# Optimization experiments

Hardware: AMD Instinct MI355X
Metric: run time of the kernel (lower is better)

Reference implementation:

```python
import jax, jax.numpy as jnp
import numpy as np

NUM_RADII, NUM_THETA = 3, 16
RADIUS = 40.0
DT = 0.1
RELU_SHIFT = 0.2
B, N, NB, T_ENC, OTHER_CH = 4, 512, 512, 16, 3


def _rot_mats():
    # bin-center angles of the num_theta angular bins
    t = (jnp.arange(NUM_THETA, dtype=jnp.float32) + 0.5) * (2.0 * jnp.pi / NUM_THETA) - jnp.pi
    c, s = jnp.cos(t), jnp.sin(t)
    return jnp.stack([jnp.stack([c, -s], -1), jnp.stack([s, c], -1)], -2)  # [T,2,2]


def _steer_kernel(W):
    # W: [R,T,O,I,2,2]; equivariant steering K[r,t] = R(theta_t) W[r,t] R(theta_t)^T
    Rm = _rot_mats()
    K = jnp.einsum('tab,rtoibc,tdc->rtoiad', Rm, W, Rm)
    return K.reshape(NUM_RADII * NUM_THETA, W.shape[2], W.shape[3], 2, 2)  # [K,O,I,2,2]


def _equi_conv(src_pos, qry_pos, feats, mask, W):
    # src_pos [B,S,2], qry_pos [B,Q,2], feats [B,S,I,2] vector features, mask [B,Q,S]
    rel = src_pos[:, None, :, :] - qry_pos[:, :, None, :]          # [B,Q,S,2]
    d2 = jnp.sum(rel * rel, -1)
    dist = jnp.sqrt(d2 + 1e-9)
    theta = jnp.arctan2(rel[..., 1], rel[..., 0])
    rb = jnp.clip((dist / RADIUS * NUM_RADII).astype(jnp.int32), 0, NUM_RADII - 1)
    tb = jnp.mod(jnp.floor((theta + jnp.pi) / (2.0 * jnp.pi) * NUM_THETA).astype(jnp.int32), NUM_THETA)
    kidx = rb * NUM_THETA + tb                                     # [B,Q,S] polar bin id
    win = jnp.maximum(1.0 - d2 / (RADIUS * RADIUS), 0.0) ** 3      # smooth radial window
    w = win * mask
    H = jax.nn.one_hot(kidx, NUM_RADII * NUM_THETA, dtype=feats.dtype) * w[..., None]  # [B,Q,S,K]
    M = jnp.einsum('bqsk,bsiv->bqkiv', H, feats)                   # bin-accumulated neighbor features
    K = _steer_kernel(W)
    return jnp.einsum('bqkiv,koiuv->bqou', M, K)                   # [B,Q,O,2]


def _equi_linear(f, A, Bm):
    # rotation-equivariant linear on vector channels: (a*I + b*J) per (out,in)
    Jf = jnp.stack([-f[..., 1], f[..., 0]], -1)
    return jnp.einsum('oi,bniv->bnov', A, f) + jnp.einsum('oi,bniv->bnov', Bm, Jf)


def _forward(p0_enc, v0_enc, p0, v0, a, other_feats, box, box_feats, fluid_mask, box_mask,
             W_cf, W_co, A_df, B_df, layer_params):
    # update_pos_vel
    v1 = v0 + DT * a
    p1 = p0 + DT * (v0 + v1) * 0.5
    # forward(): feats = cat(other_feats, v0_enc) on channel dim -2
    feats = jnp.concatenate([other_feats, v0_enc], -2)
    # compute_correction
    fluid_feats = jnp.concatenate([v1[:, :, None, :], feats], -2)  # [B,N,20,2]
    out_conv_fluid = _equi_conv(p1, p1, fluid_feats, fluid_mask, W_cf)
    out_dense_fluid = _equi_linear(fluid_feats, A_df, B_df)
    out_conv_obst = _equi_conv(box, p1, box_feats[:, :, None, :], box_mask, W_co)
    output = jnp.concatenate([out_conv_obst, out_conv_fluid, out_dense_fluid], -2)  # [B,N,48,2]
    for (Wc, Ad, Bd) in layer_params:
        mags = (jnp.sum(output * output, -1) + 1e-6)[..., None]
        in_feats = output / mags * jax.nn.relu(mags - RELU_SHIFT)
        oc = _equi_conv(p1, p1, in_feats, fluid_mask, Wc)
        od = _equi_linear(in_feats, Ad, Bd)
        if od.shape[-2] == output.shape[-2]:
            output = oc + od + output
        else:
            output = oc + od
    corr = output / 128.0                                          # [B,N,1,2]
    # apply_correction
    p_corrected = p1 + corr[..., 0, :]
    v_corrected = (p_corrected - p0) / DT
    return p_corrected, v_corrected


def setup_inputs():
    key = jax.random.key(0)
    ks = jax.random.split(key, 32)
    d = {}
    d['p0_enc'] = jax.random.normal(ks[0], (B, N, T_ENC, 2), jnp.float32)
    d['v0_enc'] = jax.random.normal(ks[1], (B, N, T_ENC, 2), jnp.float32)
    d['p0'] = jax.random.uniform(ks[2], (B, N, 2), jnp.float32) * 100.0
    d['v0'] = jax.random.normal(ks[3], (B, N, 2), jnp.float32)
    d['a'] = jax.random.normal(ks[4], (B, N, 2), jnp.float32)
    d['other_feats'] = jax.random.normal(ks[5], (B, N, OTHER_CH, 2), jnp.float32)
    d['box'] = jax.random.uniform(ks[6], (B, NB, 2), jnp.float32) * 100.0
    d['box_feats'] = jax.random.normal(ks[7], (B, NB, 2), jnp.float32)
    d['fluid_mask'] = (jax.random.uniform(ks[8], (B, N, N)) < 0.5).astype(jnp.float32)
    d['box_mask'] = (jax.random.uniform(ks[9], (B, N, NB)) < 0.5).astype(jnp.float32)
    sc = 0.05
    d['W_cf'] = sc * jax.random.normal(ks[10], (NUM_RADII, NUM_THETA, 16, 20, 2, 2), jnp.float32)
    d['W_co'] = sc * jax.random.normal(ks[11], (NUM_RADII, NUM_THETA, 16, 1, 2, 2), jnp.float32)
    d['A_df'] = sc * jax.random.normal(ks[12], (16, 20), jnp.float32)
    d['B_df'] = sc * jax.random.normal(ks[13], (16, 20), jnp.float32)
    chans = [(32, 48), (32, 32), (32, 32), (1, 32)]
    for i, (o, ci) in enumerate(chans, start=1):
        d['W_c%d' % i] = sc * jax.random.normal(ks[13 + 3 * i], (NUM_RADII, NUM_THETA, o, ci, 2, 2), jnp.float32)
        d['A_d%d' % i] = sc * jax.random.normal(ks[14 + 3 * i], (o, ci), jnp.float32)
        d['B_d%d' % i] = sc * jax.random.normal(ks[15 + 3 * i], (o, ci), jnp.float32)
    return d


def reference(p0_enc, v0_enc, p0, v0, a, other_feats, box, box_feats, fluid_mask, box_mask,
              W_cf, W_co, A_df, B_df, W_c1, A_d1, B_d1, W_c2, A_d2, B_d2,
              W_c3, A_d3, B_d3, W_c4, A_d4, B_d4):
    layer_params = [(W_c1, A_d1, B_d1), (W_c2, A_d2, B_d2), (W_c3, A_d3, B_d3), (W_c4, A_d4, B_d4)]
    return _forward(p0_enc, v0_enc, p0, v0, a, other_feats, box, box_feats, fluid_mask, box_mask,
                    W_cf, W_co, A_df, B_df, layer_params)
```

## Files before the change

kernel.cpp:

```cpp
#include <hip/hip_runtime.h>
#include <cstdint>
#include <cstddef>

#define PI_F 3.14159265358979323846f

constexpr int BB = 4, NN = 512, BN = 2048, NBIN = 48;

typedef __attribute__((ext_vector_type(8))) short v8s;
typedef __attribute__((ext_vector_type(4))) float v4f;

__device__ __forceinline__ unsigned short f2bf(float f) {
  unsigned u = __float_as_uint(f);
  unsigned r = (u + 0x7FFFu + ((u >> 16) & 1u)) >> 16;
  return (unsigned short)r;
}
__device__ __forceinline__ float bf2f(unsigned short s) {
  return __uint_as_float(((unsigned)s) << 16);
}

__device__ __forceinline__ void steer_f32(const float* __restrict__ W, float* __restrict__ K2,
                                          int O, int I, int Ipad, int idx, int total) {
  if (idx >= total) return;
  int i = idx % Ipad;
  int o = (idx / Ipad) % O;
  int k = idx / (Ipad * O);
  int CTc = O * 2;
  size_t r0 = (size_t)((k*Ipad + i)*2 + 0) * CTc + o*2;
  size_t r1 = r0 + CTc;
  if (i >= I) { K2[r0]=0.f; K2[r0+1]=0.f; K2[r1]=0.f; K2[r1+1]=0.f; return; }
  int tt = k % 16;
  float ang = (tt + 0.5f) * (2.0f * PI_F / 16.0f) - PI_F;
  float ct = cosf(ang), st = sinf(ang);
  const float* Wp = W + ((size_t)(k*O + o)*I + i) * 4;
  float w00 = Wp[0], w01 = Wp[1], w10 = Wp[2], w11 = Wp[3];
  float rw00 = ct*w00 - st*w10, rw01 = ct*w01 - st*w11;
  float rw10 = st*w00 + ct*w10, rw11 = st*w01 + ct*w11;
  K2[r0 + 0] = rw00*ct - rw01*st;
  K2[r0 + 1] = rw10*ct - rw11*st;
  K2[r1 + 0] = rw00*st + rw01*ct;
  K2[r1 + 1] = rw10*st + rw11*ct;
}

__device__ __forceinline__ void steer_bf16T(const float* __restrict__ W,
                                            unsigned short* __restrict__ K2T,
                                            int O, int I, int Ipad, int Kd,
                                            int idx, int total) {
  if (idx >= total) return;
  int i = idx % Ipad;
  int o = (idx / Ipad) % O;
  int k = idx / (Ipad * O);
  size_t c0 = (size_t)(o*2 + 0) * Kd + (k*Ipad + i)*2;
  size_t c1 = (size_t)(o*2 + 1) * Kd + (k*Ipad + i)*2;
  if (i >= I) { K2T[c0]=0; K2T[c0+1]=0; K2T[c1]=0; K2T[c1+1]=0; return; }
  int tt = k % 16;
  float ang = (tt + 0.5f) * (2.0f * PI_F / 16.0f) - PI_F;
  float ct = cosf(ang), st = sinf(ang);
  const float* Wp = W + ((size_t)(k*O + o)*I + i) * 4;
  float w00 = Wp[0], w01 = Wp[1], w10 = Wp[2], w11 = Wp[3];
  float rw00 = ct*w00 - st*w10, rw01 = ct*w01 - st*w11;
  float rw10 = st*w00 + ct*w10, rw11 = st*w01 + ct*w11;
  K2T[c0 + 0] = f2bf(rw00*ct - rw01*st);
  K2T[c0 + 1] = f2bf(rw00*st + rw01*ct);
  K2T[c1 + 0] = f2bf(rw10*ct - rw11*st);
  K2T[c1 + 1] = f2bf(rw10*st + rw11*ct);
}

__global__ __launch_bounds__(256) void setup_kernel(
    const float* __restrict__ p0, const float* __restrict__ v0,
    const float* __restrict__ a, const float* __restrict__ other,
    const float* __restrict__ v0enc, float* __restrict__ p1, float* __restrict__ F0,
    const float* Wcf, unsigned short* K2CF, const float* Wco, float* K2CO,
    const float* Wc1, unsigned short* K2C1, const float* Wc2, unsigned short* K2C2,
    const float* Wc3, unsigned short* K2C3, const float* Wc4, float* K2C4) {
  int blk = blockIdx.x;
  int t = threadIdx.x;
  if (blk < 8) {
    int n = blk * 256 + t;
    float p0x = p0[n*2], p0y = p0[n*2+1];
    float v0x = v0[n*2], v0y = v0[n*2+1];
    float ax = a[n*2],  ay = a[n*2+1];
    float v1x = v0x + 0.1f*ax, v1y = v0y + 0.1f*ay;
    p1[n*2]   = p0x + 0.1f*(v0x+v1x)*0.5f;
    p1[n*2+1] = p0y + 0.1f*(v0y+v1y)*0.5f;
    float* F = F0 + (size_t)n*48;
    F[0] = v1x; F[1] = v1y;
    for (int c = 0; c < 3; ++c) {
      F[2+c*2]   = other[(n*3+c)*2];
      F[2+c*2+1] = other[(n*3+c)*2+1];
    }
    for (int c = 0; c < 16; ++c) {
      F[8+c*2]   = v0enc[(n*16+c)*2];
      F[8+c*2+1] = v0enc[(n*16+c)*2+1];
    }
    for (int c = 40; c < 48; ++c) F[c] = 0.0f;
  } else if (blk < 80)  steer_bf16T(Wcf, K2CF, 16, 20, 24, 2304, (blk-8)*256 + t, 18432);
  else if (blk < 83)  steer_f32(Wco, K2CO, 16, 1, 1,   (blk-80)*256 + t, 768);
  else if (blk < 371) steer_bf16T(Wc1, K2C1, 32, 48, 48, 4608, (blk-83)*256 + t, 73728);
  else if (blk < 563) steer_bf16T(Wc2, K2C2, 32, 32, 32, 3072, (blk-371)*256 + t, 49152);
  else if (blk < 755) steer_bf16T(Wc3, K2C3, 32, 32, 32, 3072, (blk-563)*256 + t, 49152);
  else                steer_f32(Wc4, K2C4, 1, 32, 32,  (blk-755)*256 + t, 1536);
}

__global__ __launch_bounds__(256) void pairs_all(const float* __restrict__ qry,
                                                 const float* __restrict__ srcF,
                                                 const float* __restrict__ maskF,
                                                 float* __restrict__ wlF, int* __restrict__ plF,
                                                 int* __restrict__ cntF,
                                                 const float* __restrict__ srcO,
                                                 const float* __restrict__ maskO,
                                                 float* __restrict__ wlO, int* __restrict__ plO,
                                                 int* __restrict__ cntO) {
  bool isBox = blockIdx.x >= 512;
  int qblk = isBox ? (blockIdx.x - 512) : blockIdx.x;
  const float* src = isBox ? srcO : srcF;
  const float* mask = isBox ? maskO : maskF;
  float* wlist = isBox ? wlO : wlF;
  int* plist = isBox ? plO : plF;
  int* cnt = isBox ? cntO : cntF;

  int wv = threadIdx.x >> 6;
  int lane = threadIdx.x & 63;
  int q = qblk * 4 + wv;
  int b = q >> 9;
  float qx = qry[q*2], qy = qry[q*2+1];
  const float* sb = src + b*1024;
  const float* mb = mask + (size_t)q*512;
  float* wl = wlist + (size_t)q*512;
  int* pl = plist + (size_t)q*512;
  int base = 0;
  for (int ch = 0; ch < 8; ++ch) {
    int s = ch*64 + lane;
    float sx = sb[s*2], sy = sb[s*2+1];
    float rx = sx - qx, ry = sy - qy;
    float d2 = rx*rx + ry*ry;
    float m = mb[s];
    float wi = fmaxf(1.0f - d2 / 1600.0f, 0.0f);
    float w = wi*wi*wi*m;
    bool pred = w > 0.0f;
    int k = 0;
    if (pred) {
      float dist = sqrtf(d2 + 1e-9f);
      float theta = atan2f(ry, rx);
      int rb = (int)(dist / 40.0f * 3.0f);
      rb = rb > 2 ? 2 : rb;
      float u = (theta + PI_F) / (2.0f * PI_F) * 16.0f;
      int tb = ((int)floorf(u)) & 15;
      k = rb*16 + tb;
    }
    unsigned long long msk = __ballot(pred);
    int before = __popcll(msk & ((1ull<<lane)-1ull));
    if (pred) {
      wl[base + before] = w;
      pl[base + before] = (s<<6) | k;
    }
    base += __popcll(msk);
  }
  if (lane == 0) cnt[q] = base;
}

template<int C2>
__device__ __forceinline__ void accum_loop(float* __restrict__ M, int sw, int c, int nnz,
    const float* __restrict__ wls, const int* __restrict__ pls,
    const float* __restrict__ fb) {
  if (nnz <= 0) return;
  constexpr int W = 16;
  float wA[W], fA[W]; int kA[W];
  #pragma unroll
  for (int j = 0; j < W; ++j) {
    bool v = j < nnz;
    float wv = v ? wls[j] : 0.0f;
    int p = v ? pls[j] : 0;
    wA[j] = wv; kA[j] = (p & 63) * C2;
    fA[j] = fb[(p >> 6) * C2];
  }
  for (int base = 0; base < nnz; base += W) {
    float wB[W], fB[W]; int kB[W];
    if (base + W < nnz) {
      #pragma unroll
      for (int j = 0; j < W; ++j) {
        int idx = base + W + j;
        bool v = idx < nnz;
        float wv = v ? wls[idx] : 0.0f;
        int p = v ? pls[idx] : 0;
        wB[j] = wv; kB[j] = (p & 63) * C2;
        fB[j] = fb[(size_t)(p >> 6) * C2];
      }
    }
    asm volatile("" ::: "memory");
    #pragma unroll
    for (int j = 0; j < W; ++j) M[(kA[j] + c) ^ sw] += wA[j] * fA[j];
    #pragma unroll
    for (int j = 0; j < W; ++j) { wA[j] = wB[j]; kA[j] = kB[j]; fA[j] = fB[j]; }
  }
}

template<int QB, int TPB>
__device__ __forceinline__ void stage_lists(int q0, const int* __restrict__ csh,
    const float* __restrict__ wlist, const int* __restrict__ plist,
    float* __restrict__ wsh, int* __restrict__ psh) {
  const int t = threadIdx.x;
  for (int i = t; i < QB*128; i += TPB) {
    int qs = i >> 7, j = i & 127;
    if (j*4 < csh[qs]) {
      ((float4*)(wsh + qs*512))[j] = ((const float4*)(wlist + (size_t)(q0+qs)*512))[j];
      ((int4*)(psh + qs*512))[j]   = ((const int4*)(plist + (size_t)(q0+qs)*512))[j];
    }
  }
}

template<int C2, int QB, int TPB>
__global__ __launch_bounds__(TPB, 1) void accum4(const float* __restrict__ wlist,
                                                 const int* __restrict__ plist,
                                                 const int* __restrict__ cnt,
                                                 const float* __restrict__ feats,
                                                 unsigned short* __restrict__ Mout) {
  constexpr int Kd = NBIN * C2;
  static_assert(TPB == QB * C2, "TPB must equal QB*C2");
  __shared__ float Ml[QB * Kd];
  __shared__ float wsh[QB*512];
  __shared__ int   psh[QB*512];
  __shared__ int   csh[QB];
  const int t = threadIdx.x;
  const int q0 = blockIdx.x * QB;
  for (int i = t; i < QB*Kd; i += TPB) Ml[i] = 0.0f;
  if (t < QB) csh[t] = (q0 + t < BN) ? cnt[q0 + t] : 0;
  __syncthreads();
  stage_lists<QB, TPB>(q0, csh, wlist, plist, wsh, psh);
  __syncthreads();
  {
    const int ql = t / C2, c = t % C2;
    const int q = q0 + ql;
    accum_loop<C2>(Ml + ql*Kd, 0, c, csh[ql],
                   wsh + ql*512, psh + ql*512,
                   feats + (size_t)(q >> 9)*512*C2 + c);
  }
  __syncthreads();
  const int rows = (q0 + QB <= BN) ? QB : (BN - q0);
  unsigned* dst = (unsigned*)(Mout + (size_t)q0 * Kd);
  const float2* s2 = (const float2*)Ml;
  const int lim = rows * (Kd/2);
  for (int i = t; i < lim; i += TPB) {
    float2 v = s2[i];
    dst[i] = (unsigned)f2bf(v.x) | ((unsigned)f2bf(v.y) << 16);
  }
}

template<int CT>
__global__ __launch_bounds__(256) void gemm_mfma(const unsigned short* __restrict__ A,
                                                 const unsigned short* __restrict__ B,
                                                 float* __restrict__ G, int Kd, int kn) {
  const int lane = threadIdx.x & 63;
  const int w = threadIdx.x >> 6;
  const int mblk = blockIdx.x;
  const int ks = blockIdx.y * 4 + w;
  const int k0 = ks * kn;
  const int m = lane & 15, quad = lane >> 4;
  constexpr int NT = CT / 16;
  const unsigned short* Ar0 = A + (size_t)(mblk*32 + m) * Kd + k0 + quad*8;
  const unsigned short* Ar1 = Ar0 + (size_t)16 * Kd;
  const unsigned short* Bp[NT];
  #pragma unroll
  for (int nt = 0; nt < NT; ++nt)
    Bp[nt] = B + (size_t)(nt*16 + m) * Kd + k0 + quad*8;
  v4f acc[2][NT];
  #pragma unroll
  for (int mt = 0; mt < 2; ++mt)
    for (int nt = 0; nt < NT; ++nt)
      acc[mt][nt] = (v4f){0.0f, 0.0f, 0.0f, 0.0f};
  for (int kt = 0; kt < kn; kt += 32) {
    v8s a0 = *(const v8s*)(Ar0 + kt);
    v8s a1 = *(const v8s*)(Ar1 + kt);
    #pragma unroll
    for (int nt = 0; nt < NT; ++nt) {
      v8s bv = *(const v8s*)(Bp[nt] + kt);
      acc[0][nt] = __builtin_amdgcn_mfma_f32_16x16x32_bf16(a0, bv, acc[0][nt], 0, 0, 0);
      acc[1][nt] = __builtin_amdgcn_mfma_f32_16x16x32_bf16(a1, bv, acc[1][nt], 0, 0, 0);
    }
  }
  float* Gb = G + ((size_t)ks * BN + mblk*32) * CT;
  #pragma unroll
  for (int mt = 0; mt < 2; ++mt)
    for (int nt = 0; nt < NT; ++nt)
      for (int r = 0; r < 4; ++r)
        Gb[(mt*16 + quad*4 + r) * CT + nt*16 + m] = acc[mt][nt][r];
}

__global__ void epilogueL(const float* __restrict__ Gp, int SPLIT,
                          const float* __restrict__ inPrev, int I,
                          const float* __restrict__ Ad, const float* __restrict__ Bd,
                          const float* __restrict__ prevOut, int doRes,
                          float* __restrict__ outCur, float* __restrict__ inNext) {
  int idx = blockIdx.x * blockDim.x + threadIdx.x;
  if (idx >= BN*32) return;
  int o = idx % 32, q = idx / 32;
  float x = 0.0f, y = 0.0f;
  for (int sp = 0; sp < SPLIT; ++sp) {
    size_t base = ((size_t)sp*BN + q)*64 + o*2;
    x += Gp[base]; y += Gp[base+1];
  }
  const float* f = inPrev + (size_t)q * I * 2;
  for (int i = 0; i < I; ++i) {
    float fx = f[i*2], fy = f[i*2+1];
    float Av = Ad[o*I+i], Bv = Bd[o*I+i];
    x += Av*fx - Bv*fy;
    y += Av*fy + Bv*fx;
  }
  if (doRes) {
    x += prevOut[(size_t)idx*2];
    y += prevOut[(size_t)idx*2+1];
  }
  outCur[(size_t)idx*2]   = x;
  outCur[(size_t)idx*2+1] = y;
  float m = x*x + y*y + 1e-6f;
  float sc = fmaxf(m - 0.2f, 0.0f) / m;
  inNext[(size_t)idx*2]   = x * sc;
  inNext[(size_t)idx*2+1] = y * sc;
}

__global__ __launch_bounds__(256, 1) void fused_s0(
    const float* __restrict__ wlF, const int* __restrict__ plF, const int* __restrict__ cntF,
    const float* __restrict__ F0, const unsigned short* __restrict__ K2CF,
    const float* __restrict__ wlO, const int* __restrict__ plO, const int* __restrict__ cntO,
    const float* __restrict__ boxf, const float* __restrict__ K2CO,
    const float* __restrict__ Adf, const float* __restrict__ Bdf,
    float* __restrict__ in1) {
  constexpr int QB = 4;
  constexpr int Kd = 2304;
  constexpr int KW = 576;
  __shared__ float Ml[QB * Kd];
  __shared__ float Mo[QB * 96];
  __shared__ float red[4][QB * 32];
  __shared__ float wshF[QB*512];
  __shared__ int   pshF[QB*512];
  __shared__ float wshO[QB*512];
  __shared__ int   pshO[QB*512];
  __shared__ int cshF[QB];
  __shared__ int cshO[QB];
  const int t = threadIdx.x;
  const int q0 = blockIdx.x * QB;
  for (int i = t; i < QB*Kd; i += 256) Ml[i] = 0.0f;
  for (int i = t; i < QB*96; i += 256) Mo[i] = 0.0f;
  if (t < QB) cshF[t] = cntF[q0 + t];
  else if (t < 2*QB) cshO[t-QB] = cntO[q0 + t - QB];
  __syncthreads();
  for (int i = t; i < 2*QB*128; i += 256) {
    int half = i >> 9;
    int qs = (i >> 7) & (QB-1), j = i & 127;
    if (half == 0) {
      if (j*4 < cshF[qs]) {
        ((float4*)(wshF + qs*512))[j] = ((const float4*)(wlF + (size_t)(q0+qs)*512))[j];
        ((int4*)(pshF + qs*512))[j]   = ((const int4*)(plF + (size_t)(q0+qs)*512))[j];
      }
    } else {
      if (j*4 < cshO[qs]) {
        ((float4*)(wshO + qs*512))[j] = ((const float4*)(wlO + (size_t)(q0+qs)*512))[j];
        ((int4*)(pshO + qs*512))[j]   = ((const int4*)(plO + (size_t)(q0+qs)*512))[j];
      }
    }
  }
  __syncthreads();
  if (t < 192) {
    const int ql = t / 48, c = t % 48;
    const int q = q0 + ql;
    accum_loop<48>(Ml + ql*Kd, (ql & 3) << 2, c, cshF[ql],
                   wshF + ql*512, pshF + ql*512,
                   F0 + (size_t)(q >> 9)*512*48 + c);
  } else if (t < 200) {
    const int idx = t - 192;
    const int ql = idx >> 1, c = idx & 1;
    const int q = q0 + ql;
    accum_loop<2>(Mo + ql*96, 0, c, cshO[ql],
                  wshO + ql*512, pshO + ql*512,
                  boxf + (size_t)(q >> 9)*1024 + c);
  }
  __syncthreads();
  {
    const int lane = t & 63, w = t >> 6;
    const int m = lane & 15, quad = lane >> 4;
    const int ar = m & 3;
    const int sw = ar << 2;
    const float* Abase = Ml + ar * Kd;
    const int kb = w * KW + quad * 8;
    const unsigned short* Bb0 = K2CF + (size_t)m * Kd + kb;
    const unsigned short* Bb1 = K2CF + (size_t)(16 + m) * Kd + kb;
    v4f acc[2];
    acc[0] = (v4f){0,0,0,0}; acc[1] = (v4f){0,0,0,0};
    float4 a0c = *(const float4*)(Abase + (kb ^ sw));
    float4 a1c = *(const float4*)(Abase + ((kb + 4) ^ sw));
    v8s b0c = *(const v8s*)(Bb0);
    v8s b1c = *(const v8s*)(Bb1);
    for (int kt = 0; kt < KW; kt += 32) {
      float4 a0n, a1n; v8s b0n, b1n;
      if (kt + 32 < KW) {
        const int jn = kb + kt + 32;
        a0n = *(const float4*)(Abase + (jn ^ sw));
        a1n = *(const float4*)(Abase + ((jn + 4) ^ sw));
        b0n = *(const v8s*)(Bb0 + kt + 32);
        b1n = *(const v8s*)(Bb1 + kt + 32);
      }
      v8s av;
      av[0]=(short)f2bf(a0c.x); av[1]=(short)f2bf(a0c.y); av[2]=(short)f2bf(a0c.z); av[3]=(short)f2bf(a0c.w);
      av[4]=(short)f2bf(a1c.x); av[5]=(short)f2bf(a1c.y); av[6]=(short)f2bf(a1c.z); av[7]=(short)f2bf(a1c.w);
      acc[0] = __builtin_amdgcn_mfma_f32_16x16x32_bf16(av, b0c, acc[0], 0, 0, 0);
      acc[1] = __builtin_amdgcn_mfma_f32_16x16x32_bf16(av, b1c, acc[1], 0, 0, 0);
      a0c = a0n; a1c = a1n; b0c = b0n; b1c = b1n;
    }
    if (quad == 0) {
      #pragma unroll
      for (int nt = 0; nt < 2; ++nt)
        #pragma unroll
        for (int r = 0; r < 4; ++r)
          red[w][r*32 + nt*16 + m] = acc[nt][r];
    }
  }
  __syncthreads();
  if (t < 192) {
    const int ql = t / 48, ch = t % 48;
    const int q = q0 + ql;
    float x = 0.0f, y = 0.0f;
    if (ch < 16) {
      const float* Mq = Mo + ql*96;
      for (int j = 0; j < 96; ++j) {
        float mv = Mq[j];
        x += mv * K2CO[j*32 + ch*2];
        y += mv * K2CO[j*32 + ch*2 + 1];
      }
    } else if (ch < 32) {
      int o = ch - 16;
      x = red[0][ql*32+o*2] + red[1][ql*32+o*2] + red[2][ql*32+o*2] + red[3][ql*32+o*2];
      y = red[0][ql*32+o*2+1] + red[1][ql*32+o*2+1] + red[2][ql*32+o*2+1] + red[3][ql*32+o*2+1];
    } else {
      int o = ch - 32;
      const float* f = F0 + (size_t)q*48;
      for (int i = 0; i < 20; ++i) {
        float fx = f[i*2], fy = f[i*2+1];
        float Av = Adf[o*20+i], Bv = Bdf[o*20+i];
        x += Av*fx - Bv*fy;
        y += Av*fy + Bv*fx;
      }
    }
    float mm = x*x + y*y + 1e-6f;
    float sc = fmaxf(mm - 0.2f, 0.0f) / mm;
    size_t idx = (size_t)q*48 + ch;
    in1[idx*2]   = x * sc;
    in1[idx*2+1] = y * sc;
  }
}

template<int C2, int CT, int I, int QB>
__global__ __launch_bounds__(C2*QB, 1) void fused_layer(
    const float* __restrict__ wlist, const int* __restrict__ plist,
    const int* __restrict__ cnt, const float* __restrict__ feats,
    const unsigned short* __restrict__ K2T,
    const float* __restrict__ Ad, const float* __restrict__ Bd,
    const float* __restrict__ prevOut, int doRes,
    float* __restrict__ outCur, float* __restrict__ inNext) {
  constexpr int Kd = NBIN * C2;
  constexpr int TPB = C2 * QB;
  constexpr int NW = TPB / 64;
  constexpr int KW = Kd / NW;
  constexpr int NT = CT / 16;
  static_assert(KW % 32 == 0, "KW must be multiple of 32");
  __shared__ float Ml[QB * Kd];
  __shared__ float red[NW][QB * CT];
  __shared__ float wsh[QB*512];
  __shared__ int   psh[QB*512];
  __shared__ int csh[QB];
  const int t = threadIdx.x;
  const int q0 = blockIdx.x * QB;
  for (int i = t; i < QB*Kd; i += TPB) Ml[i] = 0.0f;
  if (t < QB) csh[t] = cnt[q0 + t];
  __syncthreads();
  stage_lists<QB, TPB>(q0, csh, wlist, plist, wsh, psh);
  __syncthreads();
  {
    const int ql = t / C2, c = t % C2;
    const int q = q0 + ql;
    accum_loop<C2>(Ml + ql*Kd, (ql & 3) << 2, c, csh[ql],
                   wsh + ql*512, psh + ql*512,
                   feats + (size_t)(q >> 9)*512*C2 + c);
  }
  __syncthreads();
  const int lane = t & 63, w = t >> 6;
  const int m = lane & 15, quad = lane >> 4;
  const int ar = m & (QB-1);
  const int sw = ar << 2;
  const float* Abase = Ml + ar * Kd;
  const int kb = w * KW + quad * 8;
  const unsigned short* Bb[NT];
  #pragma unroll
  for (int nt = 0; nt < NT; ++nt)
    Bb[nt] = K2T + (size_t)(nt*16 + m) * Kd + kb;
  v4f acc[NT];
  #pragma unroll
  for (int nt = 0; nt < NT; ++nt) acc[nt] = (v4f){0,0,0,0};
  float4 a0c = *(const float4*)(Abase + (kb ^ sw));
  float4 a1c = *(const float4*)(Abase + ((kb + 4) ^ sw));
  v8s bc[NT];
  #pragma unroll
  for (int nt = 0; nt < NT; ++nt) bc[nt] = *(const v8s*)(Bb[nt]);
  for (int kt = 0; kt < KW; kt += 32) {
    float4 a0n, a1n; v8s bn[NT];
    if (kt + 32 < KW) {
      const int jn = kb + kt + 32;
      a0n = *(const float4*)(Abase + (jn ^ sw));
      a1n = *(const float4*)(Abase + ((jn + 4) ^ sw));
      #pragma unroll
      for (int nt = 0; nt < NT; ++nt) bn[nt] = *(const v8s*)(Bb[nt] + kt + 32);
    }
    v8s av;
    av[0]=(short)f2bf(a0c.x); av[1]=(short)f2bf(a0c.y); av[2]=(short)f2bf(a0c.z); av[3]=(short)f2bf(a0c.w);
    av[4]=(short)f2bf(a1c.x); av[5]=(short)f2bf(a1c.y); av[6]=(short)f2bf(a1c.z); av[7]=(short)f2bf(a1c.w);
    #pragma unroll
    for (int nt = 0; nt < NT; ++nt)
      acc[nt] = __builtin_amdgcn_mfma_f32_16x16x32_bf16(av, bc[nt], acc[nt], 0, 0, 0);
    a0c = a0n; a1c = a1n;
    #pragma unroll
    for (int nt = 0; nt < NT; ++nt) bc[nt] = bn[nt];
  }
  if (quad == 0) {
    #pragma unroll
    for (int nt = 0; nt < NT; ++nt)
      #pragma unroll
      for (int r = 0; r < QB; ++r)
        red[w][r*CT + nt*16 + m] = acc[nt][r];
  }
  __syncthreads();
  if (t < QB * (CT/2)) {
    const int o = t % (CT/2), ql = t / (CT/2);
    const int q = q0 + ql;
    float x = 0.0f, y = 0.0f;
    #pragma unroll
    for (int w2 = 0; w2 < NW; ++w2) {
      x += red[w2][ql*CT + o*2];
      y += red[w2][ql*CT + o*2 + 1];
    }
    const float* f = feats + (size_t)q * C2;
    for (int i = 0; i < I; ++i) {
      float fx = f[i*2], fy = f[i*2+1];
      float Av = Ad[o*I + i], Bv = Bd[o*I + i];
      x += Av*fx - Bv*fy;
      y += Av*fy + Bv*fx;
    }
    size_t idx = (size_t)q * (CT/2) + o;
    if (doRes) { x += prevOut[idx*2]; y += prevOut[idx*2+1]; }
    outCur[idx*2]   = x;
    outCur[idx*2+1] = y;
    float mm = x*x + y*y + 1e-6f;
    float sc = fmaxf(mm - 0.2f, 0.0f) / mm;
    inNext[idx*2]   = x * sc;
    inNext[idx*2+1] = y * sc;
  }
}

__global__ __launch_bounds__(256, 1) void fused_l4(
    const float* __restrict__ wl, const int* __restrict__ pl, const int* __restrict__ cnt,
    const float* __restrict__ in4, const float* __restrict__ K2C4,
    const float* __restrict__ Ad4, const float* __restrict__ Bd4,
    const float* __restrict__ p1, const float* __restrict__ p0,
    float* __restrict__ dout) {
  constexpr int QB = 4, Kd = 3072;
  __shared__ float Ml[QB * Kd];
  __shared__ float wsh[QB*512];
  __shared__ int   psh[QB*512];
  __shared__ int csh[QB];
  const int t = threadIdx.x;
  const int q0 = blockIdx.x * QB;
  for (int i = t; i < QB*Kd; i += 256) Ml[i] = 0.0f;
  if (t < QB) csh[t] = cnt[q0 + t];
  __syncthreads();
  stage_lists<QB, 256>(q0, csh, wl, pl, wsh, psh);
  __syncthreads();
  {
    const int ql = t / 64, c = t % 64;
    const int q = q0 + ql;
    accum_loop<64>(Ml + ql*Kd, (ql & 3) << 2, c, csh[ql],
                   wsh + ql*512, psh + ql*512,
                   in4 + (size_t)(q >> 9)*512*64 + c);
  }
  __syncthreads();
  const int lane = t & 63, w = t >> 6;
  const int q = q0 + w;
  const int sw = (w & 3) << 2;
  const float* Mq = Ml + w*Kd;
  float a0 = 0.0f, a1 = 0.0f;
  for (int j = lane; j < Kd; j += 64) {
    float av = Mq[j ^ sw];
    a0 += av * K2C4[j*2];
    a1 += av * K2C4[j*2+1];
  }
  if (lane < 32) {
    float fx = in4[q*64 + lane*2], fy = in4[q*64 + lane*2 + 1];
    float Av = Ad4[lane], Bv = Bd4[lane];
    a0 += Av*fx - Bv*fy;
    a1 += Av*fy + Bv*fx;
  }
  for (int off = 32; off > 0; off >>= 1) {
    a0 += __shfl_down(a0, off);
    a1 += __shfl_down(a1, off);
  }
  if (lane == 0) {
    float px = p1[q*2]   + a0/128.0f;
    float py = p1[q*2+1] + a1/128.0f;
    dout[q*2] = px; dout[q*2+1] = py;
    dout[4096 + q*2]   = (px - p0[q*2]) / 0.1f;
    dout[4096 + q*2+1] = (py - p0[q*2+1]) / 0.1f;
  }
}

extern "C" void kernel_launch(void* const* d_in, const int* in_sizes, int n_in,
                              void* d_out, int out_size, void* d_ws, size_t ws_size,
                              hipStream_t stream) {
  (void)in_sizes; (void)n_in; (void)out_size; (void)ws_size;
  const float* v0_enc = (const float*)d_in[1];
  const float* p0     = (const float*)d_in[2];
  const float* v0     = (const float*)d_in[3];
  const float* a      = (const float*)d_in[4];
  const float* other  = (const float*)d_in[5];
  const float* box    = (const float*)d_in[6];
  const float* boxf   = (const float*)d_in[7];
  const float* fmask  = (const float*)d_in[8];
  const float* bmask  = (const float*)d_in[9];
  const float* Wcf = (const float*)d_in[10];
  const float* Wco = (const float*)d_in[11];
  const float* Adf = (const float*)d_in[12];
  const float* Bdf = (const float*)d_in[13];
  const float* Wc1 = (const float*)d_in[14];
  const float* Ad1 = (const float*)d_in[15];
  const float* Bd1 = (const float*)d_in[16];
  const float* Wc2 = (const float*)d_in[17];
  const float* Ad2 = (const float*)d_in[18];
  const float* Bd2 = (const float*)d_in[19];
  const float* Wc3 = (const float*)d_in[20];
  const float* Ad3 = (const float*)d_in[21];
  const float* Bd3 = (const float*)d_in[22];
  const float* Wc4 = (const float*)d_in[23];
  const float* Ad4 = (const float*)d_in[24];
  const float* Bd4 = (const float*)d_in[25];

  float* ws = (float*)d_ws;
  float* P1    = ws + 0;
  float* F0    = ws + 4096;
  unsigned short* K2CF = (unsigned short*)(ws + 102400);
  float* K2CO  = ws + 176128;
  unsigned short* K2C1 = (unsigned short*)(ws + 179200);
  unsigned short* K2C2 = (unsigned short*)(ws + 474112);
  unsigned short* K2C3 = (unsigned short*)(ws + 670720);
  float* K2C4  = ws + 867328;
  float* WFl   = ws + 873472;
  int*   PFl   = (int*)(ws + 1922048);
  int*   CNTF  = (int*)(ws + 2970624);
  int*   CNTO  = (int*)(ws + 2972672);
  float* IN1   = ws + 2974720;
  float* IN2   = ws + 3171328;
  float* IN3   = ws + 3302400;
  float* IN4   = ws + 3433472;
  float* OUTA  = ws + 3564544;
  float* OUTB  = ws + 3695616;
  float* GPART = ws + 4027392;
  unsigned short* MBUF = (unsigned short*)(ws + 6124544);
  float* WOl   = ws + 15561728;
  int*   POl   = (int*)(ws + 16610304);

  setup_kernel<<<761, 256, 0, stream>>>(p0, v0, a, other, v0_enc, P1, F0,
                                        Wcf, K2CF, Wco, K2CO, Wc1, K2C1,
                                        Wc2, K2C2, Wc3, K2C3, Wc4, K2C4);
  pairs_all<<<1024, 256, 0, stream>>>(P1, P1, fmask, WFl, PFl, CNTF,
                                      box, bmask, WOl, POl, CNTO);
  fused_s0<<<512, 256, 0, stream>>>(WFl, PFl, CNTF, F0, K2CF,
                                    WOl, POl, CNTO, boxf, K2CO, Adf, Bdf, IN1);
  accum4<96, 2, 192><<<1024, 192, 0, stream>>>(WFl, PFl, CNTF, IN1, MBUF);
  gemm_mfma<64><<<dim3(64, 4), 256, 0, stream>>>(MBUF, K2C1, GPART, 4608, 288);
  epilogueL<<<256, 256, 0, stream>>>(GPART, 16, IN1, 48, Ad1, Bd1, nullptr, 0, OUTA, IN2);
  fused_layer<64, 64, 32, 4><<<512, 256, 0, stream>>>(WFl, PFl, CNTF, IN2, K2C2,
                                                      Ad2, Bd2, OUTA, 1, OUTB, IN3);
  fused_layer<64, 64, 32, 4><<<512, 256, 0, stream>>>(WFl, PFl, CNTF, IN3, K2C3,
                                                      Ad3, Bd3, OUTB, 1, OUTA, IN4);
  fused_l4<<<512, 256, 0, stream>>>(WFl, PFl, CNTF, IN4, K2C4, Ad4, Bd4,
                                    P1, p0, (float*)d_out);
}
```

Before: 319.2 us.

## Sort neighbor lists by polar bin to accumulate in registers

The pair-building kernel now counts neighbors per bin with shared-memory histograms, scans them, and scatters each entry into a bin-sorted position using ballot-based rank matching. The accumulation loop exploits this ordering: it keeps a running register sum per bin and writes it to the shared bin buffer, replacing a read-modify-write per entry. This trades extra ballots, atomics and a scan in the pair kernel for cheaper accumulation, and it relies on the ordering being strictly by bin and on padded entries mapping to the last bin without overwriting real sums.

```diff
diff --git a/kernel.cpp b/kernel.cpp
--- a/kernel.cpp
+++ b/kernel.cpp
@@ -110,6 +110,9 @@
                                                  const float* __restrict__ maskO,
                                                  float* __restrict__ wlO, int* __restrict__ plO,
                                                  int* __restrict__ cntO) {
+  __shared__ int hist[4][48];
+  __shared__ int bstart[4][48];
+  __shared__ int runc[4][48];
   bool isBox = blockIdx.x >= 512;
   int qblk = isBox ? (blockIdx.x - 512) : blockIdx.x;
   const float* src = isBox ? srcO : srcF;
@@ -127,7 +130,11 @@
   const float* mb = mask + (size_t)q*512;
   float* wl = wlist + (size_t)q*512;
   int* pl = plist + (size_t)q*512;
-  int base = 0;
+
+  if (lane < 48) { hist[wv][lane] = 0; runc[wv][lane] = 0; }
+
+  float wreg[8]; int kreg[8];
+  unsigned char predreg[8];
   for (int ch = 0; ch < 8; ++ch) {
     int s = ch*64 + lane;
     float sx = sb[s*2], sy = sb[s*2+1];
@@ -137,7 +144,7 @@
     float wi = fmaxf(1.0f - d2 / 1600.0f, 0.0f);
     float w = wi*wi*wi*m;
     bool pred = w > 0.0f;
-    int k = 0;
+    int k = 63;
     if (pred) {
       float dist = sqrtf(d2 + 1e-9f);
       float theta = atan2f(ry, rx);
@@ -146,16 +153,42 @@
       float u = (theta + PI_F) / (2.0f * PI_F) * 16.0f;
       int tb = ((int)floorf(u)) & 15;
       k = rb*16 + tb;
-    }
-    unsigned long long msk = __ballot(pred);
-    int before = __popcll(msk & ((1ull<<lane)-1ull));
+      atomicAdd(&hist[wv][k], 1);
+    }
+    wreg[ch] = w; kreg[ch] = k; predreg[ch] = pred ? 1 : 0;
+  }
+  int cntv = (lane < 48) ? hist[wv][lane] : 0;
+  int sc = cntv;
+  #pragma unroll
+  for (int off = 1; off < 64; off <<= 1) {
+    int o = __shfl_up(sc, off);
+    if (lane >= off) sc += o;
+  }
+  if (lane < 48) bstart[wv][lane] = sc - cntv;
+  if (lane == 47) cnt[q] = sc;
+
+  for (int ch = 0; ch < 8; ++ch) {
+    bool pred = predreg[ch] != 0;
+    int k = kreg[ch];
+    float w = wreg[ch];
+    unsigned long long mEq = __ballot(pred);
+    #pragma unroll
+    for (int bit = 0; bit < 6; ++bit) {
+      unsigned long long mbm = __ballot((k >> bit) & 1);
+      mEq &= ((k >> bit) & 1) ? mbm : ~mbm;
+    }
+    int rank = __popcll(mEq & ((1ull<<lane)-1ull));
+    int total = __popcll(mEq);
     if (pred) {
-      wl[base + before] = w;
-      pl[base + before] = (s<<6) | k;
-    }
-    base += __popcll(msk);
-  }
-  if (lane == 0) cnt[q] = base;
+      int bs = bstart[wv][k];
+      int rc = runc[wv][k];
+      int pos = bs + rc + rank;
+      int s = ch*64 + lane;
+      wl[pos] = w;
+      pl[pos] = (s<<6) | k;
+      if (rank == total - 1) runc[wv][k] = rc + total;
+    }
+  }
 }
 
 template<int C2>
@@ -169,10 +202,12 @@
   for (int j = 0; j < W; ++j) {
     bool v = j < nnz;
     float wv = v ? wls[j] : 0.0f;
-    int p = v ? pls[j] : 0;
-    wA[j] = wv; kA[j] = (p & 63) * C2;
+    int p = v ? pls[j] : 47;
+    wA[j] = wv; kA[j] = p & 63;
     fA[j] = fb[(p >> 6) * C2];
   }
+  int kcur = -1;
+  float acc = 0.0f;
   for (int base = 0; base < nnz; base += W) {
     float wB[W], fB[W]; int kB[W];
     if (base + W < nnz) {
@@ -181,14 +216,18 @@
         int idx = base + W + j;
         bool v = idx < nnz;
         float wv = v ? wls[idx] : 0.0f;
-        int p = v ? pls[idx] : 0;
-        wB[j] = wv; kB[j] = (p & 63) * C2;
+        int p = v ? pls[idx] : 47;
+        wB[j] = wv; kB[j] = p & 63;
         fB[j] = fb[(size_t)(p >> 6) * C2];
       }
     }
     asm volatile("" ::: "memory");
     #pragma unroll
-    for (int j = 0; j < W; ++j) M[(kA[j] + c) ^ sw] += wA[j] * fA[j];
+    for (int j = 0; j < W; ++j) {
+      acc = (kA[j] == kcur ? acc : 0.0f) + wA[j] * fA[j];
+      kcur = kA[j];
+      M[(kcur * C2 + c) ^ sw] = acc;
+    }
     #pragma unroll
     for (int j = 0; j < W; ++j) { wA[j] = wB[j]; kA[j] = kB[j]; fA[j] = fB[j]; }
   }
```

New measurement: 312.6 us. -2.1%, faster.
